# Kernel optimization log

Measured on AMD Instinct MI355X. Metric: run time of the kernel, lower is better.

## Reference

```python
import jax, jax.numpy as jnp
import numpy as np

EPS = 1e-6
NUM_HEADS = 8


def _phi(x):
    # positive feature map: elu(x) + 1
    return jax.nn.elu(x) + 1.0


def setup_inputs() -> dict:
    key = jax.random.key(0)
    k1, k2, k3, k4, k5 = jax.random.split(key, 5)
    B, T, J, d = 8, 2048, 17, 128
    x = jax.random.normal(k1, (B, T, J, d + 1), dtype=jnp.float32)
    # qkv projection on the spatial part (xavier-ish small init, gain 0.02)
    w_qkv = jax.random.normal(k2, (3 * d, d), dtype=jnp.float32) * 0.02
    b_qkv = jnp.zeros((3 * d,), dtype=jnp.float32)
    # LorentzLinear out projection (spatial d -> d, time recomputed)
    w_out = jax.random.normal(k3, (d, d), dtype=jnp.float32) * (1.0 / np.sqrt(d))
    b_out = jnp.zeros((d,), dtype=jnp.float32)
    return {"x": x, "w_qkv": w_qkv, "b_qkv": b_qkv, "w_out": w_out, "b_out": b_out}


def reference(x, w_qkv, b_qkv, w_out, b_out):
    B, T, J, D = x.shape
    d = D - 1
    H = NUM_HEADS
    d_h = d // H
    BJ = B * J

    # [B,T,J,D] -> [BJ, T, D], drop the time coordinate
    x_flat = jnp.transpose(x, (0, 2, 1, 3)).reshape(BJ, T, D)
    x_spatial = x_flat[..., 1:]                                  # [BJ, T, d]

    qkv = x_spatial @ w_qkv.T + b_qkv                            # [BJ, T, 3d]
    qkv = qkv.reshape(BJ, T, 3, H, d_h)
    q = jnp.transpose(qkv[:, :, 0], (0, 2, 1, 3))                # [BJ, H, T, d_h]
    k = jnp.transpose(qkv[:, :, 1], (0, 2, 1, 3))
    v = jnp.transpose(qkv[:, :, 2], (0, 2, 1, 3))

    q_m = _phi(q)
    k_m = _phi(k)

    # linear attention: phi(K)^T V outer product, then phi(Q) aggregation
    kv = jnp.einsum("bhtd,bhte->bhde", k_m, v)                   # [BJ,H,d_h,d_h]
    agg = jnp.einsum("bhtd,bhde->bhte", q_m, kv)                 # [BJ,H,T,d_h]

    k_sum = k_m.sum(axis=2)                                      # [BJ,H,d_h]
    z_denom = jnp.einsum("bhtd,bhd->bht", q_m, k_sum)
    z_denom = jnp.clip(z_denom, EPS, None)[..., None]            # [BJ,H,T,1]
    agg = agg / z_denom

    agg_flat = jnp.transpose(agg, (0, 2, 1, 3)).reshape(BJ, T, d)
    sq = jnp.clip((agg_flat * agg_flat).sum(-1, keepdims=True), EPS, None)
    agg_time = jnp.sqrt(1.0 + sq)
    z = jnp.concatenate([agg_time, agg_flat], axis=-1)           # [BJ, T, D]

    # LorentzLinear out projection: linear on spatial part, recompute time
    y = z[..., 1:] @ w_out.T + b_out                             # [BJ, T, d]
    y_time = jnp.sqrt(1.0 + (y * y).sum(-1, keepdims=True))
    z = jnp.concatenate([y_time, y], axis=-1)                    # [BJ, T, D]

    z = z.reshape(B, J, T, D)
    return jnp.transpose(z, (0, 2, 1, 3))                        # [B, T, J, D]
```

## Files before the change

kernel.cpp:

```cpp
#include <hip/hip_runtime.h>
#include <hip/hip_bf16.h>
#include <math.h>

#define B_   8
#define T_   2048
#define J_   17
#define D_   129
#define d_   128
#define H_   8
#define BJ_  (B_ * J_)
#define EPS_ 1e-6f

#define CHK  8
#define RPBK (T_ / CHK)
#define NITK (RPBK / 64)
#define CHO  8
#define RPBO (T_ / CHO)
#define NITO (RPBO / 64)

typedef short bf8 __attribute__((ext_vector_type(8)));
typedef float fx4 __attribute__((ext_vector_type(4)));

__device__ __forceinline__ float phi_f(float x) {
    return x > 0.f ? x + 1.f : __expf(x);
}
__device__ __forceinline__ short f2b(float f) {
    __hip_bfloat16 h = __float2bfloat16(f);
    return *reinterpret_cast<short*>(&h);
}
__device__ __forceinline__ unsigned f2b2(float lo, float hi) {
    float2 p; p.x = lo; p.y = hi;
    __hip_bfloat162 h2 = __float22bfloat162_rn(p);
    return *reinterpret_cast<unsigned*>(&h2);
}
__device__ __forceinline__ float b2f(short s) {
    union { float f; unsigned u; } c;
    c.u = ((unsigned)(unsigned short)s) << 16;
    return c.f;
}
__device__ __forceinline__ bf8 ld_w8(const float* p) {
    const float4* q = reinterpret_cast<const float4*>(p);
    float4 a = q[0], b = q[1];
    bf8 t;
    unsigned* tu = reinterpret_cast<unsigned*>(&t);
    tu[0] = f2b2(a.x, a.y); tu[1] = f2b2(a.z, a.w);
    tu[2] = f2b2(b.x, b.y); tu[3] = f2b2(b.z, b.w);
    return t;
}

__global__ __launch_bounds__(256) void pass_kv(
        const float* __restrict__ x,
        const float* __restrict__ wqkv, const float* __restrict__ bqkv,
        float* __restrict__ kvw,
        float* __restrict__ ksw) {
    const int bj = blockIdx.y, b = bj / J_, j = bj % J_;
    const int t0 = blockIdx.x * RPBK;
    const int tid = threadIdx.x, wave = tid >> 6, lane = tid & 63;
    const int quad = lane >> 4, l16 = lane & 15;
    const int rsw = (l16 & 7) << 4;

    __shared__ __align__(16) short sx[64 * 128];
    __shared__ __align__(16) short kT[128 * 64];
    __shared__ __align__(16) short vT[128 * 64];

    bf8 wf[4][4];
    float bias[4];
    #pragma unroll
    for (int nt = 0; nt < 4; ++nt) {
        const int n = d_ + wave * 64 + nt * 16 + l16;
        bias[nt] = bqkv[n];
        #pragma unroll
        for (int ks = 0; ks < 4; ++ks)
            wf[nt][ks] = ld_w8(wqkv + (size_t)n * d_ + ks * 32 + quad * 8);
    }

    fx4 kva[2];
    kva[0] = (fx4){0.f, 0.f, 0.f, 0.f};
    kva[1] = (fx4){0.f, 0.f, 0.f, 0.f};
    float ksp[4] = {0.f, 0.f, 0.f, 0.f};

    for (int it = 0; it < NITK; ++it) {
        const int tb = t0 + it * 64;
        {
            #pragma unroll
            for (int i = 0; i < 16; ++i) {
                const int F = tid + 256 * i, row = F >> 6, c2 = F & 63;
                const float* xr = x + ((size_t)((b * T_ + tb + row) * J_ + j)) * D_ + 1 + 2 * c2;
                *reinterpret_cast<unsigned*>(reinterpret_cast<char*>(sx) +
                    row * 256 + ((c2 * 4) ^ ((row & 7) << 4))) = f2b2(xr[0], xr[1]);
            }
        }
        __syncthreads();

        short* dst = (wave < 2) ? kT : vT;
        const int fbase = (wave & 1) * 64;
        const bool isk = (wave < 2);

        #pragma unroll
        for (int pr = 0; pr < 2; ++pr) {
            fx4 acc[2][4];
            #pragma unroll
            for (int n2 = 0; n2 < 2; ++n2)
                #pragma unroll
                for (int mt = 0; mt < 4; ++mt) acc[n2][mt] = (fx4){0.f, 0.f, 0.f, 0.f};

            #pragma unroll
            for (int ks = 0; ks < 4; ++ks) {
                bf8 af[4];
                #pragma unroll
                for (int mt = 0; mt < 4; ++mt)
                    af[mt] = *reinterpret_cast<const bf8*>(
                        reinterpret_cast<char*>(sx) + (mt * 16 + l16) * 256 +
                        ((ks * 64 + quad * 16) ^ rsw));
                #pragma unroll
                for (int n2 = 0; n2 < 2; ++n2)
                    #pragma unroll
                    for (int mt = 0; mt < 4; ++mt)
                        acc[n2][mt] = __builtin_amdgcn_mfma_f32_16x16x32_bf16(
                            af[mt], wf[pr * 2 + n2][ks], acc[n2][mt], 0, 0, 0);
            }

            #pragma unroll
            for (int n2 = 0; n2 < 2; ++n2) {
                const int nt = pr * 2 + n2;
                const int feat = fbase + nt * 16 + l16;
                #pragma unroll
                for (int mt = 0; mt < 4; ++mt) {
                    float v0 = acc[n2][mt][0] + bias[nt];
                    float v1 = acc[n2][mt][1] + bias[nt];
                    float v2 = acc[n2][mt][2] + bias[nt];
                    float v3 = acc[n2][mt][3] + bias[nt];
                    if (isk) {
                        v0 = phi_f(v0); v1 = phi_f(v1);
                        v2 = phi_f(v2); v3 = phi_f(v3);
                        ksp[nt] += (v0 + v1) + (v2 + v3);
                    }
                    const unsigned lo = f2b2(v0, v1), hi = f2b2(v2, v3);
                    *reinterpret_cast<unsigned long long*>(
                        reinterpret_cast<char*>(dst) + feat * 128 +
                        ((mt * 32 + quad * 8) ^ rsw)) =
                        (unsigned long long)lo | ((unsigned long long)hi << 32);
                }
            }
        }
        __syncthreads();

        #pragma unroll
        for (int hh = 0; hh < 2; ++hh) {
            const int h = wave * 2 + hh;
            const int feat = h * 16 + l16;
            #pragma unroll
            for (int ks2 = 0; ks2 < 2; ++ks2) {
                bf8 ak = *reinterpret_cast<const bf8*>(
                    reinterpret_cast<char*>(kT) + feat * 128 +
                    ((ks2 * 64 + quad * 16) ^ rsw));
                bf8 bv = *reinterpret_cast<const bf8*>(
                    reinterpret_cast<char*>(vT) + feat * 128 +
                    ((ks2 * 64 + quad * 16) ^ rsw));
                kva[hh] = __builtin_amdgcn_mfma_f32_16x16x32_bf16(ak, bv, kva[hh], 0, 0, 0);
            }
        }
    }

    #pragma unroll
    for (int hh = 0; hh < 2; ++hh) {
        const int h = wave * 2 + hh;
        float* p = kvw + (((size_t)bj * H_ + h) * 16 + l16) * 16 + quad * 4;
        #pragma unroll
        for (int r = 0; r < 4; ++r) atomicAdd(p + r, kva[hh][r]);
    }
    if (wave < 2) {
        #pragma unroll
        for (int nt = 0; nt < 4; ++nt) {
            float s = ksp[nt];
            s += __shfl_xor(s, 16);
            s += __shfl_xor(s, 32);
            if (lane < 16)
                atomicAdd(ksw + (size_t)bj * d_ + wave * 64 + nt * 16 + l16, s);
        }
    }
}

__global__ __launch_bounds__(256, 2) void pass_out(
        const float* __restrict__ x,
        const float* __restrict__ wqkv, const float* __restrict__ bqkv,
        const float* __restrict__ wout, const float* __restrict__ bout,
        const float* __restrict__ kvw, const float* __restrict__ ksw,
        float* __restrict__ out) {
    const int bj = blockIdx.y, b = bj / J_, j = bj % J_;
    const int t0 = blockIdx.x * RPBO;
    const int tid = threadIdx.x, wave = tid >> 6, lane = tid & 63;
    const int quad = lane >> 4, l16 = lane & 15;
    const int rsw = (l16 & 7) << 4;

    __shared__ __align__(16) short sxg[64 * 128];
    __shared__ __align__(16) short qm[64 * 136];
    __shared__ __align__(16) short kvT2[H_ * 2 * 16 * 8];
    __shared__ __align__(16) short ksshi[d_];
    __shared__ __align__(16) short ksslo[d_];
    __shared__ float rnorm[64];

    bf8 wqf[2][4], wof[2][4];
    float bq2[2], bo2[2];
    #pragma unroll
    for (int nt = 0; nt < 2; ++nt) {
        const int n = wave * 32 + nt * 16 + l16;
        bq2[nt] = bqkv[n];
        bo2[nt] = bout[n];
        #pragma unroll
        for (int ks = 0; ks < 4; ++ks) {
            wqf[nt][ks] = ld_w8(wqkv + (size_t)n * d_ + ks * 32 + quad * 8);
            wof[nt][ks] = ld_w8(wout + (size_t)n * d_ + ks * 32 + quad * 8);
        }
    }
    #pragma unroll
    for (int u = 0; u < 8; ++u) {
        const int lin = tid + 256 * u;
        const int jj = lin & 7, jv = (lin >> 3) & 15, qd = (lin >> 7) & 1, h = lin >> 8;
        kvT2[lin] = f2b(kvw[(((size_t)bj * H_ + h) * 16 + jv) * 16 + qd * 8 + jj]);
    }
    if (tid < d_) {
        const float v = ksw[(size_t)bj * d_ + tid];
        const short hi = f2b(v);
        ksshi[tid] = hi;
        ksslo[tid] = f2b(v - b2f(hi));
    }
    if (tid < 64) rnorm[tid] = 0.f;

    for (int it = 0; it < NITO; ++it) {
        const int tb = t0 + it * 64;
        {
            #pragma unroll
            for (int i = 0; i < 16; ++i) {
                const int F = tid + 256 * i, row = F >> 6, c2 = F & 63;
                const float* xr = x + ((size_t)((b * T_ + tb + row) * J_ + j)) * D_ + 1 + 2 * c2;
                *reinterpret_cast<unsigned*>(reinterpret_cast<char*>(sxg) +
                    row * 256 + ((c2 * 4) ^ ((row & 7) << 4))) = f2b2(xr[0], xr[1]);
            }
        }
        __syncthreads();

        fx4 acc[2][4];
        #pragma unroll
        for (int nt = 0; nt < 2; ++nt)
            #pragma unroll
            for (int mt = 0; mt < 4; ++mt) acc[nt][mt] = (fx4){0.f, 0.f, 0.f, 0.f};
        #pragma unroll
        for (int ks = 0; ks < 4; ++ks) {
            bf8 af[4];
            #pragma unroll
            for (int mt = 0; mt < 4; ++mt)
                af[mt] = *reinterpret_cast<const bf8*>(
                    reinterpret_cast<char*>(sxg) + (mt * 16 + l16) * 256 +
                    ((ks * 64 + quad * 16) ^ rsw));
            #pragma unroll
            for (int nt = 0; nt < 2; ++nt)
                #pragma unroll
                for (int mt = 0; mt < 4; ++mt)
                    acc[nt][mt] = __builtin_amdgcn_mfma_f32_16x16x32_bf16(
                        af[mt], wqf[nt][ks], acc[nt][mt], 0, 0, 0);
        }
        #pragma unroll
        for (int nt = 0; nt < 2; ++nt) {
            const int col = wave * 32 + nt * 16 + l16;
            #pragma unroll
            for (int mt = 0; mt < 4; ++mt)
                #pragma unroll
                for (int r = 0; r < 4; ++r)
                    qm[(mt * 16 + quad * 4 + r) * 136 + col] =
                        f2b(phi_f(acc[nt][mt][r] + bq2[nt]));
        }
        asm volatile("" ::: "memory");

        #pragma unroll
        for (int hh = 0; hh < 2; ++hh) {
            const int h = wave * 2 + hh;
            bf8 bk = (bf8){0, 0, 0, 0, 0, 0, 0, 0};
            bf8 bh = (bf8){0, 0, 0, 0, 0, 0, 0, 0};
            bf8 bl = (bf8){0, 0, 0, 0, 0, 0, 0, 0};
            if (quad < 2) {
                bk = *reinterpret_cast<const bf8*>(&kvT2[((h * 2 + quad) * 16 + l16) * 8]);
                bh = *reinterpret_cast<const bf8*>(&ksshi[h * 16 + quad * 8]);
                bl = *reinterpret_cast<const bf8*>(&ksslo[h * 16 + quad * 8]);
            }
            #pragma unroll
            for (int mt = 0; mt < 4; ++mt) {
                bf8 aq = (bf8){0, 0, 0, 0, 0, 0, 0, 0};
                if (quad < 2)
                    aq = *reinterpret_cast<const bf8*>(
                        &qm[(mt * 16 + l16) * 136 + h * 16 + quad * 8]);
                fx4 ag = __builtin_amdgcn_mfma_f32_16x16x32_bf16(
                    aq, bk, (fx4){0.f, 0.f, 0.f, 0.f}, 0, 0, 0);
                fx4 dd = __builtin_amdgcn_mfma_f32_16x16x32_bf16(
                    aq, bl, (fx4){0.f, 0.f, 0.f, 0.f}, 0, 0, 0);
                dd = __builtin_amdgcn_mfma_f32_16x16x32_bf16(aq, bh, dd, 0, 0, 0);
                #pragma unroll
                for (int r = 0; r < 4; ++r) {
                    const float rin = __builtin_amdgcn_rcpf(fmaxf(dd[r], EPS_));
                    qm[(mt * 16 + quad * 4 + r) * 136 + h * 16 + l16] =
                        f2b(ag[r] * rin);
                }
            }
        }
        __syncthreads();

        fx4 ya[2][4];
        #pragma unroll
        for (int nt = 0; nt < 2; ++nt)
            #pragma unroll
            for (int mt = 0; mt < 4; ++mt) ya[nt][mt] = (fx4){0.f, 0.f, 0.f, 0.f};
        #pragma unroll
        for (int ks = 0; ks < 4; ++ks) {
            bf8 af[4];
            #pragma unroll
            for (int mt = 0; mt < 4; ++mt)
                af[mt] = *reinterpret_cast<const bf8*>(
                    &qm[(mt * 16 + l16) * 136 + ks * 32 + quad * 8]);
            #pragma unroll
            for (int nt = 0; nt < 2; ++nt)
                #pragma unroll
                for (int mt = 0; mt < 4; ++mt)
                    ya[nt][mt] = __builtin_amdgcn_mfma_f32_16x16x32_bf16(
                        af[mt], wof[nt][ks], ya[nt][mt], 0, 0, 0);
        }

        #pragma unroll
        for (int mt = 0; mt < 4; ++mt) {
            float sq[4] = {0.f, 0.f, 0.f, 0.f};
            #pragma unroll
            for (int nt = 0; nt < 2; ++nt) {
                const int col = wave * 32 + nt * 16 + l16;
                #pragma unroll
                for (int r = 0; r < 4; ++r) {
                    const float y = ya[nt][mt][r] + bo2[nt];
                    const int t = tb + mt * 16 + quad * 4 + r;
                    out[((size_t)(b * T_ + t) * J_ + j) * D_ + 1 + col] = y;
                    sq[r] += y * y;
                }
            }
            #pragma unroll
            for (int r = 0; r < 4; ++r) {
                float s = sq[r];
                s += __shfl_xor(s, 1);
                s += __shfl_xor(s, 2);
                s += __shfl_xor(s, 4);
                s += __shfl_xor(s, 8);
                if (l16 == 0) atomicAdd(&rnorm[mt * 16 + quad * 4 + r], s);
            }
        }
        __syncthreads();
        if (tid < 64) {
            const int t = tb + tid;
            out[((size_t)(b * T_ + t) * J_ + j) * D_] = sqrtf(1.f + rnorm[tid]);
            rnorm[tid] = 0.f;
        }
    }
}

extern "C" void kernel_launch(void* const* d_in, const int* in_sizes, int n_in,
                              void* d_out, int out_size, void* d_ws, size_t ws_size,
                              hipStream_t stream) {
    const float* x     = (const float*)d_in[0];
    const float* wqkv  = (const float*)d_in[1];
    const float* bqkv  = (const float*)d_in[2];
    const float* wout  = (const float*)d_in[3];
    const float* bout  = (const float*)d_in[4];
    float* out = (float*)d_out;

    float* kvw = (float*)d_ws;
    float* ksw = kvw + (size_t)BJ_ * H_ * 16 * 16;
    const size_t zero_bytes =
        ((size_t)BJ_ * H_ * 16 * 16 + (size_t)BJ_ * d_) * sizeof(float);
    hipMemsetAsync(d_ws, 0, zero_bytes, stream);

    dim3 blk(256);
    dim3 grdK(CHK, BJ_);
    dim3 grdO(CHO, BJ_);
    hipLaunchKernelGGL(pass_kv, grdK, blk, 0, stream, x, wqkv, bqkv, kvw, ksw);
    hipLaunchKernelGGL(pass_out, grdO, blk, 0, stream, x, wqkv, bqkv, wout, bout,
                       kvw, ksw, out);
}
```

Baseline: 373.2 us.

## Stash bf16-packed spatial x in workspace for second pass to load directly into LDS

The first pass now writes its swizzled bf16 tile of the spatial input to a workspace buffer. The second pass reads that buffer with global_load_lds straight into shared memory, so it no longer re-reads the strided fp32 x and converts it. This halves the second-pass input bytes and removes the uncoalesced stride-129 reads. In exchange the first pass does extra global writes, and the path is only taken when the workspace is large enough (about 71 MB).

```diff
diff --git a/kernel.cpp b/kernel.cpp
--- a/kernel.cpp
+++ b/kernel.cpp
@@ -20,6 +20,8 @@
 
 typedef short bf8 __attribute__((ext_vector_type(8)));
 typedef float fx4 __attribute__((ext_vector_type(4)));
+typedef const __attribute__((address_space(1))) unsigned char guc;
+typedef __attribute__((address_space(3))) unsigned char luc;
 
 __device__ __forceinline__ float phi_f(float x) {
     return x > 0.f ? x + 1.f : __expf(x);
@@ -52,7 +54,9 @@
         const float* __restrict__ x,
         const float* __restrict__ wqkv, const float* __restrict__ bqkv,
         float* __restrict__ kvw,
-        float* __restrict__ ksw) {
+        float* __restrict__ ksw,
+        char* __restrict__ xbg,
+        const int packed) {
     const int bj = blockIdx.y, b = bj / J_, j = bj % J_;
     const int t0 = blockIdx.x * RPBK;
     const int tid = threadIdx.x, wave = tid >> 6, lane = tid & 63;
@@ -91,6 +95,17 @@
             }
         }
         __syncthreads();
+
+        if (packed) {
+            char* dst = xbg + ((size_t)(bj * 32) + (tb >> 6)) * 16384;
+            const char* s = reinterpret_cast<const char*>(sx);
+            #pragma unroll
+            for (int u = 0; u < 4; ++u) {
+                const int off = (tid + 256 * u) * 16;
+                *reinterpret_cast<bf8*>(dst + off) =
+                    *reinterpret_cast<const bf8*>(s + off);
+            }
+        }
 
         short* dst = (wave < 2) ? kT : vT;
         const int fbase = (wave & 1) * 64;
@@ -186,6 +201,7 @@
         const float* __restrict__ wqkv, const float* __restrict__ bqkv,
         const float* __restrict__ wout, const float* __restrict__ bout,
         const float* __restrict__ kvw, const float* __restrict__ ksw,
+        const char* __restrict__ xbg, const int packed,
         float* __restrict__ out) {
     const int bj = blockIdx.y, b = bj / J_, j = bj % J_;
     const int t0 = blockIdx.x * RPBO;
@@ -229,7 +245,15 @@
 
     for (int it = 0; it < NITO; ++it) {
         const int tb = t0 + it * 64;
-        {
+        if (packed) {
+            const char* gsrc = xbg + ((size_t)(bj * 32) + (tb >> 6)) * 16384
+                             + (size_t)(wave * 4) * 1024 + (size_t)lane * 16;
+            char* lbase = reinterpret_cast<char*>(sxg) + wave * 4096;
+            #pragma unroll
+            for (int c = 0; c < 4; ++c)
+                __builtin_amdgcn_global_load_lds(
+                    (guc*)(gsrc + c * 1024), (luc*)(lbase + c * 1024), 16, 0, 0);
+        } else {
             #pragma unroll
             for (int i = 0; i < 16; ++i) {
                 const int F = tid + 256 * i, row = F >> 6, c2 = F & 63;
@@ -373,10 +397,15 @@
         ((size_t)BJ_ * H_ * 16 * 16 + (size_t)BJ_ * d_) * sizeof(float);
     hipMemsetAsync(d_ws, 0, zero_bytes, stream);
 
+    char* xbg = (char*)d_ws + zero_bytes;
+    const size_t xbg_bytes = (size_t)BJ_ * 32 * 16384;
+    const int packed = (ws_size >= zero_bytes + xbg_bytes) ? 1 : 0;
+
     dim3 blk(256);
     dim3 grdK(CHK, BJ_);
     dim3 grdO(CHO, BJ_);
-    hipLaunchKernelGGL(pass_kv, grdK, blk, 0, stream, x, wqkv, bqkv, kvw, ksw);
+    hipLaunchKernelGGL(pass_kv, grdK, blk, 0, stream, x, wqkv, bqkv, kvw, ksw,
+                       xbg, packed);
     hipLaunchKernelGGL(pass_out, grdO, blk, 0, stream, x, wqkv, bqkv, wout, bout,
-                       kvw, ksw, out);
-}
+                       kvw, ksw, xbg, packed, out);
+}
```

New measurement: 449.7 us. 1.2x slower.
